# Kernel tuning notes

Hardware: AMD Instinct MI355X
Metric: run time of the kernel (lower is better)

## Reference

```python
import jax, jax.numpy as jnp
import numpy as np

N, D_IN, D_H, D_OUT, M = 256, 768, 768, 512, 100000


def setup_inputs() -> dict:
    key = jax.random.key(0)
    ks = jax.random.split(key, 8)
    img_feats = jax.random.normal(ks[0], (N, D_IN), dtype=jnp.float32)
    w1 = jax.random.normal(ks[1], (D_H, D_IN), dtype=jnp.float32) * (1.0 / np.sqrt(D_IN))
    b1 = jax.random.normal(ks[2], (D_H,), dtype=jnp.float32) * 0.01
    w2 = jax.random.normal(ks[3], (D_OUT, D_H), dtype=jnp.float32) * (1.0 / np.sqrt(D_H))
    b2 = jax.random.normal(ks[4], (D_OUT,), dtype=jnp.float32) * 0.01
    logit_scale = jnp.asarray(np.log(1.0 / 0.07), dtype=jnp.float32)
    loc = jax.random.normal(ks[5], (M, D_OUT), dtype=jnp.float32)
    loc_feats = loc / jnp.linalg.norm(loc, axis=1, keepdims=True)  # pre-normalized gallery
    gps_gallery = jax.random.uniform(ks[6], (M, 2), dtype=jnp.float32, minval=-90.0, maxval=90.0)
    return {
        "img_feats": img_feats, "w1": w1, "b1": b1, "w2": w2, "b2": b2,
        "logit_scale": logit_scale, "loc_feats": loc_feats,
        "gps_gallery": gps_gallery, "top_k": 5,
    }


def reference(img_feats, w1, b1, w2, b2, logit_scale, loc_feats, gps_gallery, top_k):
    # Tsfm MLP head: Linear -> ReLU -> Linear
    h = jax.nn.relu(img_feats @ w1.T + b1)            # [N, D_H]
    img = h @ w2.T + b2                               # [N, D_OUT]
    # F.normalize(dim=1)
    img_n = img / jnp.linalg.norm(img, axis=1, keepdims=True)
    # forward_cached: scaled cosine-similarity logits against 100K gallery
    logits = jnp.exp(logit_scale) * (img_n @ loc_feats.T)  # [N, M]
    # predict: softmax over full gallery row, then top-k retrieval
    probs = jax.nn.softmax(logits, axis=-1)
    top_vals, top_idx = jax.lax.top_k(probs, top_k)   # [N, k]
    top_pred_gps = gps_gallery[top_idx[0]]            # [k, 2] (first image, as in original)
    top_pred_prob = top_vals[0]                       # [k]
    return (logits, top_pred_gps, top_pred_prob)
```

## Files before the change

kernel.cpp:

```cpp
#include <hip/hip_runtime.h>
#include <math.h>

#define N_IMG 256
#define DIN   768
#define DH    768
#define DOUT  512
#define M_GAL 100000
#define CAP   2048
#define MT    1568

typedef __bf16 bf16_t;
typedef __bf16 bf16x8 __attribute__((ext_vector_type(8)));
typedef float  f32x4  __attribute__((ext_vector_type(4)));
typedef float  f32x16 __attribute__((ext_vector_type(16)));

#define OFF_H      0
#define OFF_IMG    (N_IMG*DH)
#define OFF_IMGN   (OFF_IMG  + N_IMG*DOUT)
#define OFF_IMGT   (OFF_IMGN + N_IMG*DOUT)
#define OFF_STATS  (OFF_IMGT + N_IMG*DOUT/2)
#define OFF_CIDX   (OFF_STATS + 4)
#define OFF_CVAL   (OFF_CIDX + CAP)

#define OUT_GPS  ((size_t)N_IMG * (size_t)M_GAL)
#define OUT_PROB (OUT_GPS + 10)

__device__ inline unsigned fkey(float x) {
  unsigned u = __float_as_uint(x);
  return (u & 0x80000000u) ? ~u : (u | 0x80000000u);
}
__device__ inline float fkey_inv(unsigned k) {
  unsigned u = (k & 0x80000000u) ? (k ^ 0x80000000u) : ~k;
  return __uint_as_float(u);
}

template<int KDIM, int NCOLS, bool RELU>
__global__ __launch_bounds__(256) void mlp_gemm(const float* __restrict__ A,
    const float* __restrict__ B, const float* __restrict__ bias,
    float* __restrict__ C, unsigned* stats_init) {
  if (stats_init && blockIdx.x == 0 && blockIdx.y == 0 && threadIdx.x == 0) {
    stats_init[0] = 0u; stats_init[1] = 0u; stats_init[2] = 0u;
  }
  __shared__ float As[32][34];
  __shared__ float Bs[32][34];
  const int t  = threadIdx.x;
  const int rowbase = blockIdx.y * 32;
  const int colbase = blockIdx.x * 32;
  const int sm = t >> 3;
  const int kc = (t & 7) << 2;
  const int ty = t >> 4, tx = t & 15;
  float a00 = 0.f, a01 = 0.f, a10 = 0.f, a11 = 0.f;
  for (int kt = 0; kt < KDIM; kt += 32) {
    float4 av = *(const float4*)(A + (size_t)(rowbase + sm) * KDIM + kt + kc);
    float4 bv = *(const float4*)(B + (size_t)(colbase + sm) * KDIM + kt + kc);
    __syncthreads();
    As[kc+0][sm] = av.x; As[kc+1][sm] = av.y; As[kc+2][sm] = av.z; As[kc+3][sm] = av.w;
    Bs[kc+0][sm] = bv.x; Bs[kc+1][sm] = bv.y; Bs[kc+2][sm] = bv.z; Bs[kc+3][sm] = bv.w;
    __syncthreads();
#pragma unroll
    for (int j = 0; j < 32; ++j) {
      float2 a = *(const float2*)(&As[j][2*ty]);
      float2 b = *(const float2*)(&Bs[j][2*tx]);
      a00 = fmaf(a.x, b.x, a00); a01 = fmaf(a.x, b.y, a01);
      a10 = fmaf(a.y, b.x, a10); a11 = fmaf(a.y, b.y, a11);
    }
  }
  const int r0 = rowbase + 2*ty;
  const int c0 = colbase + 2*tx;
  const float bb0 = bias[c0], bb1 = bias[c0+1];
  float v00 = a00 + bb0, v01 = a01 + bb1, v10 = a10 + bb0, v11 = a11 + bb1;
  if (RELU) {
    v00 = fmaxf(v00, 0.f); v01 = fmaxf(v01, 0.f);
    v10 = fmaxf(v10, 0.f); v11 = fmaxf(v11, 0.f);
  }
  C[(size_t)r0*NCOLS + c0]       = v00; C[(size_t)r0*NCOLS + c0 + 1]     = v01;
  C[(size_t)(r0+1)*NCOLS + c0]   = v10; C[(size_t)(r0+1)*NCOLS + c0 + 1] = v11;
}

__global__ __launch_bounds__(256) void norm_cast_kernel(const float* __restrict__ img,
    float* __restrict__ img_n, bf16_t* __restrict__ img_t) {
  const int row = blockIdx.x, t = threadIdx.x;
  const float v0 = img[row*DOUT + t];
  const float v1 = img[row*DOUT + 256 + t];
  float s = v0*v0 + v1*v1;
  for (int o = 32; o > 0; o >>= 1) s += __shfl_down(s, o);
  __shared__ float ws4[4];
  if ((t & 63) == 0) ws4[t >> 6] = s;
  __syncthreads();
  const float tot = ws4[0] + ws4[1] + ws4[2] + ws4[3];
  const float inv = 1.0f / sqrtf(tot);
  const float n0 = v0 * inv, n1 = v1 * inv;
  img_n[row*DOUT + t]       = n0;
  img_n[row*DOUT + 256 + t] = n1;
  const int k0 = t, k1 = t + 256;
  img_t[(((k0 >> 3)*N_IMG) + row)*8 + (k0 & 7)] = (bf16_t)n0;
  img_t[(((k1 >> 3)*N_IMG) + row)*8 + (k1 & 7)] = (bf16_t)n1;
}

__global__ __launch_bounds__(256, 5) void logits_kernel(const float* __restrict__ loc,
    const bf16_t* __restrict__ img_t, const float* __restrict__ ls,
    float* __restrict__ out, float* __restrict__ sumexp, unsigned* __restrict__ maxkey) {
  __shared__ bf16_t Asl[8 * 128 * 8];
  __shared__ bf16_t Bsl[8 * 64 * 8];
  const int t = threadIdx.x;
  const int w = t >> 6, l = t & 63;
  const int wi = w >> 1;
  const int wc = w & 1;
  const int hi = l >> 5;
  const int lo = l & 31;
  const int bx = blockIdx.x;
  const int mtile = (bx & 7) + (bx >> 4) * 8;
  const int h     = (bx >> 3) & 1;
  const int mb = mtile * 64;
  const int m  = mb + wc * 32 + lo;

  const int sk8 = t & 7, sr0 = t >> 3;
  const int gr0 = min(mb + sr0,      M_GAL - 1);
  const int gr1 = min(mb + 32 + sr0, M_GAL - 1);
  const float* sp0 = loc + (size_t)gr0 * 512 + sk8 * 8;
  const float* sp1 = loc + (size_t)gr1 * 512 + sk8 * 8;
  bf16_t* bw0 = Bsl + (sk8 * 64 + (sr0 ^ sk8)) * 8;
  bf16_t* bw1 = bw0 + 32 * 8;

  f32x16 acc[2];
  acc[0] = (f32x16)(0.f);
  acc[1] = (f32x16)(0.f);

  float4 r00, r01, r10, r11;

#define BLOAD(c_) {                                                   \
    const float* p0_ = sp0 + (c_) * 64;                               \
    const float* p1_ = sp1 + (c_) * 64;                               \
    r00 = *(const float4*)p0_; r01 = *(const float4*)(p0_ + 4);       \
    r10 = *(const float4*)p1_; r11 = *(const float4*)(p1_ + 4);       \
  }

#define BWRITE() {                                                    \
    bf16x8 b0_, b1_;                                                  \
    b0_[0] = (bf16_t)r00.x; b0_[1] = (bf16_t)r00.y;                   \
    b0_[2] = (bf16_t)r00.z; b0_[3] = (bf16_t)r00.w;                   \
    b0_[4] = (bf16_t)r01.x; b0_[5] = (bf16_t)r01.y;                   \
    b0_[6] = (bf16_t)r01.z; b0_[7] = (bf16_t)r01.w;                   \
    b1_[0] = (bf16_t)r10.x; b1_[1] = (bf16_t)r10.y;                   \
    b1_[2] = (bf16_t)r10.z; b1_[3] = (bf16_t)r10.w;                   \
    b1_[4] = (bf16_t)r11.x; b1_[5] = (bf16_t)r11.y;                   \
    b1_[6] = (bf16_t)r11.z; b1_[7] = (bf16_t)r11.w;                   \
    *(bf16x8*)bw0 = b0_;                                              \
    *(bf16x8*)bw1 = b1_;                                              \
  }

#define STAGEA(c_) {                                                  \
    _Pragma("unroll")                                                 \
    for (int r_ = 0; r_ < 4; ++r_) {                                  \
      __builtin_amdgcn_global_load_lds(                               \
          (__attribute__((address_space(1))) void*)(img_t + (((size_t)((c_) * 8 + r_ * 2 + (t >> 7)) * 256 + h * 128 + (t & 127))) * 8), \
          (__attribute__((address_space(3))) void*)(Asl + (r_ * 256 + t) * 8), \
          16, 0, 0);                                                  \
    } }

#define COMPUTE(kt) {                                                 \
    const int kl_ = ((kt) & 3) * 2 + hi;   \
    bf16x8 af_[2];                                                    \
    _Pragma("unroll")                                                 \
    for (int i_ = 0; i_ < 2; ++i_)                                    \
      af_[i_] = *(const bf16x8*)(Asl + (kl_ * 128 + wi * 64 + i_ * 32 + lo) * 8); \
    const bf16x8 bf_ = *(const bf16x8*)(Bsl + (kl_ * 64 + ((wc * 32 + lo) ^ kl_)) * 8); \
    _Pragma("unroll")                                                 \
    for (int i_ = 0; i_ < 2; ++i_)                                    \
      acc[i_] = __builtin_amdgcn_mfma_f32_32x32x16_bf16(af_[i_], bf_, acc[i_], 0, 0, 0); \
  }

  BLOAD(0);
  STAGEA(0);
  BWRITE();
  __syncthreads();

#pragma unroll
  for (int c = 0; c < 8; ++c) {
    if (c < 7) { BLOAD(c + 1); }
#pragma unroll
    for (int q = 0; q < 4; ++q) {
      COMPUTE(c * 4 + q);
    }
    if (c < 7) {
      __syncthreads();
      STAGEA(c + 1);
      BWRITE();
      __syncthreads();
    }
  }
#undef BLOAD
#undef BWRITE
#undef STAGEA
#undef COMPUTE

  const float scale = expf(ls[0]);
  if (h == 0 && wi == 0) {
    float mx = -1e30f, se = 0.f;
    if (hi == 0 && m < M_GAL) {
      const float v = scale * acc[0][0];
      mx = v;
      se = expf(v);
    }
#pragma unroll
    for (int o = 1; o < 64; o <<= 1) {
      mx = fmaxf(mx, __shfl_xor(mx, o));
      se += __shfl_xor(se, o);
    }
    if (l == 0) { atomicAdd(sumexp, se); atomicMax(maxkey, fkey(mx)); }
  }
  if (m < M_GAL) {
#pragma unroll
    for (int i = 0; i < 2; ++i) {
      const int ib = h * 128 + wi * 64 + i * 32 + hi * 4;
#pragma unroll
      for (int r = 0; r < 16; ++r) {
        const int img = ib + (r & 3) + 8 * (r >> 2);
        out[(size_t)img * M_GAL + m] = scale * acc[i][r];
      }
    }
  }
}

__global__ __launch_bounds__(256) void collect_kernel(const float* __restrict__ out,
    const unsigned* __restrict__ maxkey, unsigned* __restrict__ counter,
    int* __restrict__ cidx) {
  const int i = blockIdx.x * 256 + threadIdx.x;
  if (i >= M_GAL) return;
  const float thresh = fkey_inv(*maxkey) - 0.8f;
  if (out[i] > thresh) {
    const unsigned p = atomicAdd(counter, 1u);
    if (p < CAP) cidx[p] = i;
  }
}

__global__ __launch_bounds__(256) void recompute_kernel(const float* __restrict__ loc,
    const float* __restrict__ img_n, const float* __restrict__ ls,
    const unsigned* __restrict__ counter, const int* __restrict__ cidx,
    float* __restrict__ cval) {
  const int w = threadIdx.x >> 6, l = threadIdx.x & 63;
  const unsigned cnt = *counter;
  const int n = (int)(cnt < CAP ? cnt : CAP);
  const float scale = expf(ls[0]);
  for (int c = blockIdx.x * 4 + w; c < n; c += gridDim.x * 4) {
    const int idx = cidx[c];
    const float* B = loc + (size_t)idx * 512;
    float s = 0.f;
#pragma unroll
    for (int e = 0; e < 8; ++e) s = fmaf(img_n[l + e*64], B[l + e*64], s);
    for (int o = 32; o > 0; o >>= 1) s += __shfl_down(s, o);
    if (l == 0) cval[c] = scale * s;
  }
}

__global__ __launch_bounds__(256) void finalize_kernel(const unsigned* __restrict__ counter,
    const int* __restrict__ cidx, const float* __restrict__ cval,
    const float* __restrict__ gps, const float* __restrict__ sumexp,
    float* __restrict__ out) {
  __shared__ float v[CAP];
  __shared__ int   id[CAP];
  __shared__ float rv[256];
  __shared__ int   ri[256];
  __shared__ int   rs[256];
  const int t = threadIdx.x;
  const unsigned cnt = *counter;
  const int n = (int)(cnt < CAP ? cnt : CAP);
  for (int i = t; i < CAP; i += 256) {
    v[i]  = (i < n) ? cval[i] : -1e30f;
    id[i] = (i < n) ? cidx[i] : 0x7fffffff;
  }
  const float se = *sumexp;
  __syncthreads();
  for (int k = 0; k < 5; ++k) {
    float bv = -1e30f; int bidx = 0x7fffffff; int bslot = -1;
    for (int i = t; i < CAP; i += 256) {
      const float vi = v[i]; const int ii = id[i];
      if (vi > bv || (vi == bv && ii < bidx)) { bv = vi; bidx = ii; bslot = i; }
    }
    rv[t] = bv; ri[t] = bidx; rs[t] = bslot;
    __syncthreads();
    for (int s = 128; s > 0; s >>= 1) {
      if (t < s) {
        if (rv[t+s] > rv[t] || (rv[t+s] == rv[t] && ri[t+s] < ri[t])) {
          rv[t] = rv[t+s]; ri[t] = ri[t+s]; rs[t] = rs[t+s];
        }
      }
      __syncthreads();
    }
    if (t == 0) {
      const int sl = rs[0]; const int gi = ri[0]; const float lv = rv[0];
      float g0 = 0.f, g1 = 0.f, pr = 0.f;
      if (sl >= 0 && gi != 0x7fffffff) {
        g0 = gps[(size_t)gi*2]; g1 = gps[(size_t)gi*2 + 1];
        pr = expf(lv) / se;
        v[sl] = -1e30f; id[sl] = 0x7fffffff;
      }
      out[OUT_GPS + 2*k]     = g0;
      out[OUT_GPS + 2*k + 1] = g1;
      out[OUT_PROB + k]      = pr;
    }
    __syncthreads();
  }
}

extern "C" void kernel_launch(void* const* d_in, const int* in_sizes, int n_in,
                              void* d_out, int out_size, void* d_ws, size_t ws_size,
                              hipStream_t stream) {
  const float* img_feats = (const float*)d_in[0];
  const float* w1  = (const float*)d_in[1];
  const float* b1  = (const float*)d_in[2];
  const float* w2  = (const float*)d_in[3];
  const float* b2  = (const float*)d_in[4];
  const float* ls  = (const float*)d_in[5];
  const float* loc = (const float*)d_in[6];
  const float* gps = (const float*)d_in[7];
  float* out = (float*)d_out;
  float* ws  = (float*)d_ws;

  float*    h       = ws + OFF_H;
  float*    img     = ws + OFF_IMG;
  float*    img_n   = ws + OFF_IMGN;
  bf16_t*   img_t   = (bf16_t*)(ws + OFF_IMGT);
  float*    sumexp  = ws + OFF_STATS;
  unsigned* maxkey  = (unsigned*)(ws + OFF_STATS + 1);
  unsigned* counter = (unsigned*)(ws + OFF_STATS + 2);
  int*      cidx    = (int*)(ws + OFF_CIDX);
  float*    cval    = ws + OFF_CVAL;

  mlp_gemm<DIN, DH, true><<<dim3(DH/32, N_IMG/32), 256, 0, stream>>>(
      img_feats, w1, b1, h, (unsigned*)(ws + OFF_STATS));
  mlp_gemm<DH, DOUT, false><<<dim3(DOUT/32, N_IMG/32), 256, 0, stream>>>(
      h, w2, b2, img, nullptr);
  norm_cast_kernel<<<N_IMG, 256, 0, stream>>>(img, img_n, img_t);
  logits_kernel<<<MT * 2, 256, 0, stream>>>(loc, img_t, ls, out, sumexp, maxkey);
  collect_kernel<<<(M_GAL + 255) / 256, 256, 0, stream>>>(out, maxkey, counter, cidx);
  recompute_kernel<<<128, 256, 0, stream>>>(loc, img_n, ls, counter, cidx, cval);
  finalize_kernel<<<1, 256, 0, stream>>>(counter, cidx, cval, gps, sumexp, out);
}
```

Baseline: 429.0 us.

## Read A fragments from global, double-buffer B in LDS, nontemporal logits stores

Drops LDS staging of the normalized image matrix; each lane now loads its A fragments directly from global memory, relying on cache since the A data is small and shared. The gallery tile is double-buffered in LDS, which removes one barrier per K-chunk. Logits stores become nontemporal to avoid polluting cache with the large output. Direct global A loads add latency inside the MFMA loop and increase per-wave global traffic.

```diff
diff --git a/kernel.cpp b/kernel.cpp
--- a/kernel.cpp
+++ b/kernel.cpp
@@ -100,8 +100,7 @@
 __global__ __launch_bounds__(256, 5) void logits_kernel(const float* __restrict__ loc,
     const bf16_t* __restrict__ img_t, const float* __restrict__ ls,
     float* __restrict__ out, float* __restrict__ sumexp, unsigned* __restrict__ maxkey) {
-  __shared__ bf16_t Asl[8 * 128 * 8];
-  __shared__ bf16_t Bsl[8 * 64 * 8];
+  __shared__ bf16_t Bsl[2 * 8 * 64 * 8];
   const int t = threadIdx.x;
   const int w = t >> 6, l = t & 63;
   const int wi = w >> 1;
@@ -122,6 +121,8 @@
   bf16_t* bw0 = Bsl + (sk8 * 64 + (sr0 ^ sk8)) * 8;
   bf16_t* bw1 = bw0 + 32 * 8;
 
+  const bf16_t* ap = img_t + (size_t)(h * 128 + wi * 64 + lo) * 8;
+
   f32x16 acc[2];
   acc[0] = (f32x16)(0.f);
   acc[1] = (f32x16)(0.f);
@@ -135,7 +136,7 @@
     r10 = *(const float4*)p1_; r11 = *(const float4*)(p1_ + 4);       \
   }
 
-#define BWRITE() {                                                    \
+#define BWRITE(pb_) {                                                 \
     bf16x8 b0_, b1_;                                                  \
     b0_[0] = (bf16_t)r00.x; b0_[1] = (bf16_t)r00.y;                   \
     b0_[2] = (bf16_t)r00.z; b0_[3] = (bf16_t)r00.w;                   \
@@ -145,53 +146,42 @@
     b1_[2] = (bf16_t)r10.z; b1_[3] = (bf16_t)r10.w;                   \
     b1_[4] = (bf16_t)r11.x; b1_[5] = (bf16_t)r11.y;                   \
     b1_[6] = (bf16_t)r11.z; b1_[7] = (bf16_t)r11.w;                   \
-    *(bf16x8*)bw0 = b0_;                                              \
-    *(bf16x8*)bw1 = b1_;                                              \
-  }
-
-#define STAGEA(c_) {                                                  \
-    _Pragma("unroll")                                                 \
-    for (int r_ = 0; r_ < 4; ++r_) {                                  \
-      __builtin_amdgcn_global_load_lds(                               \
-          (__attribute__((address_space(1))) void*)(img_t + (((size_t)((c_) * 8 + r_ * 2 + (t >> 7)) * 256 + h * 128 + (t & 127))) * 8), \
-          (__attribute__((address_space(3))) void*)(Asl + (r_ * 256 + t) * 8), \
-          16, 0, 0);                                                  \
-    } }
-
-#define COMPUTE(kt) {                                                 \
+    *(bf16x8*)(bw0 + (pb_) * 4096) = b0_;                             \
+    *(bf16x8*)(bw1 + (pb_) * 4096) = b1_;                             \
+  }
+
+#define COMPUTE(kt, pb_) {                                            \
+    const int kg_ = (kt) * 2 + hi;              \
     const int kl_ = ((kt) & 3) * 2 + hi;   \
     bf16x8 af_[2];                                                    \
     _Pragma("unroll")                                                 \
     for (int i_ = 0; i_ < 2; ++i_)                                    \
-      af_[i_] = *(const bf16x8*)(Asl + (kl_ * 128 + wi * 64 + i_ * 32 + lo) * 8); \
-    const bf16x8 bf_ = *(const bf16x8*)(Bsl + (kl_ * 64 + ((wc * 32 + lo) ^ kl_)) * 8); \
+      af_[i_] = *(const bf16x8*)(ap + ((size_t)kg_ * 256 + i_ * 32) * 8); \
+    const bf16x8 bf_ = *(const bf16x8*)(Bsl + ((pb_) * 4096 + (kl_ * 64 + ((wc * 32 + lo) ^ kl_)) * 8)); \
     _Pragma("unroll")                                                 \
     for (int i_ = 0; i_ < 2; ++i_)                                    \
       acc[i_] = __builtin_amdgcn_mfma_f32_32x32x16_bf16(af_[i_], bf_, acc[i_], 0, 0, 0); \
   }
 
   BLOAD(0);
-  STAGEA(0);
-  BWRITE();
+  BWRITE(0);
   __syncthreads();
 
 #pragma unroll
   for (int c = 0; c < 8; ++c) {
+    const int pb = c & 1;
     if (c < 7) { BLOAD(c + 1); }
 #pragma unroll
     for (int q = 0; q < 4; ++q) {
-      COMPUTE(c * 4 + q);
+      COMPUTE(c * 4 + q, pb);
     }
     if (c < 7) {
-      __syncthreads();
-      STAGEA(c + 1);
-      BWRITE();
+      BWRITE(pb ^ 1);
       __syncthreads();
     }
   }
 #undef BLOAD
 #undef BWRITE
-#undef STAGEA
 #undef COMPUTE
 
   const float scale = expf(ls[0]);
@@ -216,7 +206,7 @@
 #pragma unroll
       for (int r = 0; r < 16; ++r) {
         const int img = ib + (r & 3) + 8 * (r >> 2);
-        out[(size_t)img * M_GAL + m] = scale * acc[i][r];
+        __builtin_nontemporal_store(scale * acc[i][r], out + (size_t)img * M_GAL + m);
       }
     }
   }
```

Result: slower. 455.7 us (+6.2%).
